# Kernel optimization log

Measured on AMD Instinct MI355X. Metric: run time of the kernel, lower is better.

## Reference

```python
import jax, jax.numpy as jnp
import numpy as np

N = 100000   # nodes
M = 32       # stencil size
D = 3        # vector-field components
B = 8        # batch


def setup_inputs() -> dict:
    key = jax.random.key(0)
    k1, k2, k3 = jax.random.split(key, 3)
    fs = jax.random.normal(k1, (B, N, D), dtype=jnp.float32)
    weights = jax.random.normal(k2, (N, D, M), dtype=jnp.float32)
    stencil_indices = jax.random.randint(k3, (N, M), 0, N, dtype=jnp.int64)
    return {"fs": fs, "weights": weights, "stencil_indices": stencil_indices}


def reference(fs, weights, stencil_indices):
    # Original casts to float64; we keep float32 (jax x64 disabled by default).
    # Handle the single-field case the same way as the module.
    if fs.ndim == 2:
        fs = fs[None, ...]
    # Gather stencil neighbor values: [b, n, m, d]
    stencil_vals = fs[:, stencil_indices, :]
    # Weighted contraction over stencil (m) and component (d) dims -> [b, n]
    return jnp.einsum('ndm,bnmd->bn', weights, stencil_vals)
```

## Files before the change

kernel.cpp:

```cpp
#include <hip/hip_runtime.h>

#define N_PTS   100000
#define M_ST    32
#define D_DIM   3
#define B_BATCH 8


__device__ __forceinline__ ushort f32_to_bf16_rne(float x) {
    unsigned u = __float_as_uint(x);
    unsigned r = u + 0x7fffu + ((u >> 16) & 1u);
    return (ushort)(r >> 16);
}

__global__ __launch_bounds__(256) void transpose_fs_kernel(
    const float* __restrict__ fs,
    uint2*       __restrict__ fst)
{
    int t = blockIdx.x * blockDim.x + threadIdx.x;
    int j = t >> 3;
    int b = t & 7;
    const float* f = fs + ((size_t)b * N_PTS + (size_t)j) * 3;
    float f0 = f[0];
    float f1 = f[1];
    float f2 = f[2];
    uint2 v;
    v.x = (unsigned)f32_to_bf16_rne(f0) | ((unsigned)f32_to_bf16_rne(f1) << 16);
    v.y = (unsigned)f32_to_bf16_rne(f2);
    fst[(size_t)j * B_BATCH + b] = v;
}

__global__ __launch_bounds__(256) void rbffd_div_kernel(
    const uint2* __restrict__ fst,
    const float* __restrict__ weights,
    const int*   __restrict__ idx,
    float*       __restrict__ out)
{
    int t = blockIdx.x * blockDim.x + threadIdx.x;
    int n = t >> 3;
    int b = t & 7;

    const float* wrow = weights + (size_t)n * (D_DIM * M_ST);
    const int*   irow = idx     + (size_t)n * M_ST;

    float acc = 0.0f;
    #pragma unroll
    for (int m = 0; m < M_ST; ++m) {
        int j = irow[m];
        uint2 v = fst[(size_t)j * B_BATCH + b];
        float f0 = __uint_as_float(v.x << 16);
        float f1 = __uint_as_float(v.x & 0xffff0000u);
        float f2 = __uint_as_float(v.y << 16);
        acc = fmaf(wrow[m],      f0, acc);
        acc = fmaf(wrow[32 + m], f1, acc);
        acc = fmaf(wrow[64 + m], f2, acc);
    }

    out[(size_t)b * N_PTS + n] = acc;
}

extern "C" void kernel_launch(void* const* d_in, const int* in_sizes, int n_in,
                              void* d_out, int out_size, void* d_ws, size_t ws_size,
                              hipStream_t stream) {
    const float* fs      = (const float*)d_in[0];
    const float* weights = (const float*)d_in[1];
    const int*   idx     = (const int*)d_in[2];
    float*       out     = (float*)d_out;

    uint2* fst = (uint2*)d_ws;

    const int total  = B_BATCH * N_PTS;
    const int block  = 256;
    const int blocks = (total + block - 1) / block;

    transpose_fs_kernel<<<blocks, block, 0, stream>>>(fs, fst);
    rbffd_div_kernel  <<<blocks, block, 0, stream>>>(fst, weights, idx, out);
}
```

Before: 129.1 us.

## Process two batches per thread with 16-byte gathers and vectorized weight loads

The gather kernel now assigns 4 threads per node, and each thread handles two batch entries. Each neighbor is read as one 16-byte uint4 covering two batches, and the weights and indices are read as float4/int4 vectors. This halves the thread count and the redundant weight and index loads per node, and widens the gather transactions. In exchange each thread carries more registers, and the unroll of 2 may limit how many loads are in flight.

```diff
diff --git a/kernel.cpp b/kernel.cpp
--- a/kernel.cpp
+++ b/kernel.cpp
@@ -11,6 +11,9 @@
     unsigned r = u + 0x7fffu + ((u >> 16) & 1u);
     return (ushort)(r >> 16);
 }
+
+__device__ __forceinline__ float bf_lo(unsigned x) { return __uint_as_float(x << 16); }
+__device__ __forceinline__ float bf_hi(unsigned x) { return __uint_as_float(x & 0xffff0000u); }
 
 __global__ __launch_bounds__(256) void transpose_fs_kernel(
     const float* __restrict__ fs,
@@ -30,32 +33,66 @@
 }
 
 __global__ __launch_bounds__(256) void rbffd_div_kernel(
-    const uint2* __restrict__ fst,
+    const uint4* __restrict__ fst4,
     const float* __restrict__ weights,
     const int*   __restrict__ idx,
     float*       __restrict__ out)
 {
     int t = blockIdx.x * blockDim.x + threadIdx.x;
-    int n = t >> 3;
-    int b = t & 7;
+    int n = t >> 2;
+    int l = t & 3;
+    if (n >= N_PTS) return;
 
     const float* wrow = weights + (size_t)n * (D_DIM * M_ST);
     const int*   irow = idx     + (size_t)n * M_ST;
 
-    float acc = 0.0f;
-    #pragma unroll
-    for (int m = 0; m < M_ST; ++m) {
-        int j = irow[m];
-        uint2 v = fst[(size_t)j * B_BATCH + b];
-        float f0 = __uint_as_float(v.x << 16);
-        float f1 = __uint_as_float(v.x & 0xffff0000u);
-        float f2 = __uint_as_float(v.y << 16);
-        acc = fmaf(wrow[m],      f0, acc);
-        acc = fmaf(wrow[32 + m], f1, acc);
-        acc = fmaf(wrow[64 + m], f2, acc);
+    float acc0 = 0.0f;
+    float acc1 = 0.0f;
+
+    #pragma unroll 2
+    for (int mc = 0; mc < 8; ++mc) {
+        int4   ji = *(const int4*)  (irow + mc * 4);
+        float4 w0 = *(const float4*)(wrow +  0 + mc * 4);
+        float4 w1 = *(const float4*)(wrow + 32 + mc * 4);
+        float4 w2 = *(const float4*)(wrow + 64 + mc * 4);
+
+        uint4 g0 = fst4[(size_t)ji.x * 4 + l];
+        uint4 g1 = fst4[(size_t)ji.y * 4 + l];
+        uint4 g2 = fst4[(size_t)ji.z * 4 + l];
+        uint4 g3 = fst4[(size_t)ji.w * 4 + l];
+
+        acc0 = fmaf(w0.x, bf_lo(g0.x), acc0);
+        acc0 = fmaf(w1.x, bf_hi(g0.x), acc0);
+        acc0 = fmaf(w2.x, bf_lo(g0.y), acc0);
+        acc1 = fmaf(w0.x, bf_lo(g0.z), acc1);
+        acc1 = fmaf(w1.x, bf_hi(g0.z), acc1);
+        acc1 = fmaf(w2.x, bf_lo(g0.w), acc1);
+
+        acc0 = fmaf(w0.y, bf_lo(g1.x), acc0);
+        acc0 = fmaf(w1.y, bf_hi(g1.x), acc0);
+        acc0 = fmaf(w2.y, bf_lo(g1.y), acc0);
+        acc1 = fmaf(w0.y, bf_lo(g1.z), acc1);
+        acc1 = fmaf(w1.y, bf_hi(g1.z), acc1);
+        acc1 = fmaf(w2.y, bf_lo(g1.w), acc1);
+
+        acc0 = fmaf(w0.z, bf_lo(g2.x), acc0);
+        acc0 = fmaf(w1.z, bf_hi(g2.x), acc0);
+        acc0 = fmaf(w2.z, bf_lo(g2.y), acc0);
+        acc1 = fmaf(w0.z, bf_lo(g2.z), acc1);
+        acc1 = fmaf(w1.z, bf_hi(g2.z), acc1);
+        acc1 = fmaf(w2.z, bf_lo(g2.w), acc1);
+
+        acc0 = fmaf(w0.w, bf_lo(g3.x), acc0);
+        acc0 = fmaf(w1.w, bf_hi(g3.x), acc0);
+        acc0 = fmaf(w2.w, bf_lo(g3.y), acc0);
+        acc1 = fmaf(w0.w, bf_lo(g3.z), acc1);
+        acc1 = fmaf(w1.w, bf_hi(g3.z), acc1);
+        acc1 = fmaf(w2.w, bf_lo(g3.w), acc1);
     }
 
-    out[(size_t)b * N_PTS + n] = acc;
+    int b0 = 2 * l;
+    out[(size_t)b0       * N_PTS + n] = acc0;
+    out[(size_t)(b0 + 1) * N_PTS + n] = acc1;
 }
 
 extern "C" void kernel_launch(void* const* d_in, const int* in_sizes, int n_in,
@@ -70,8 +107,11 @@
 
     const int total  = B_BATCH * N_PTS;
     const int block  = 256;
-    const int blocks = (total + block - 1) / block;
+    const int tblocks = (total + block - 1) / block;
 
-    transpose_fs_kernel<<<blocks, block, 0, stream>>>(fs, fst);
-    rbffd_div_kernel  <<<blocks, block, 0, stream>>>(fst, weights, idx, out);
+    transpose_fs_kernel<<<tblocks, block, 0, stream>>>(fs, fst);
+
+    const int gthreads = 4 * N_PTS;
+    const int gblocks  = (gthreads + block - 1) / block;
+    rbffd_div_kernel<<<gblocks, block, 0, stream>>>((const uint4*)fst, weights, idx, out);
 }
```

After: 157.5 us. 21.9% more time.
